# Optimization experiments

Hardware: AMD Instinct MI355X
Metric: run time of the kernel (lower is better)

## Reference

```python
import jax, jax.numpy as jnp
import numpy as np

B, S, E, H = 4, 2048, 768, 12
D = E // H  # head_dim = 64


def setup_inputs() -> dict:
    key = jax.random.key(0)
    k1, k2, k3 = jax.random.split(key, 3)
    x = jax.random.normal(k1, (B, S, E), dtype=jnp.float32)
    # torch Linear(E, 3E): weight [3E, E]; we store transposed [E, 3E] for x @ W
    W_qkv = jax.random.normal(k2, (E, 3 * E), dtype=jnp.float32) * (E ** -0.5)
    b_qkv = jax.random.normal(k3, (3 * E,), dtype=jnp.float32) * 0.02
    return {"x": x, "W_qkv": W_qkv, "b_qkv": b_qkv}


def reference(x, W_qkv, b_qkv):
    n, length, embed_dim = x.shape
    qkv = x @ W_qkv + b_qkv                                   # [B, S, 3E]
    qkv = qkv.reshape(n, length, 3, H, D).transpose(2, 0, 3, 1, 4)  # [3, B, H, S, D]
    q, k, v = qkv[0], qkv[1], qkv[2]
    scores = jnp.einsum('bhsd,bhtd->bhst', q, k) * (D ** -0.5)  # [B, H, S, S]
    attn = jax.nn.softmax(scores, axis=-1)
    out = jnp.einsum('bhst,bhtd->bhsd', attn, v)               # [B, H, S, D]
    return out.transpose(0, 2, 1, 3).reshape(n, length, embed_dim)
```

## Files before the change

### kernel.cpp

```cpp
#include <hip/hip_runtime.h>
#include <cmath>

#define B_ 4
#define S_ 2048
#define E_ 768
#define H_ 12
#define D_ 64
#define NE3 (3*E_)
#define QKV_ELEMS ((size_t)B_*H_*S_*D_)

typedef __attribute__((ext_vector_type(8)))  short bf16x8;
typedef __attribute__((ext_vector_type(4)))  float f32x4;
typedef __attribute__((ext_vector_type(16))) float f32x16;

__device__ __forceinline__ unsigned short f2bf(float f) {
    union { float f; unsigned u; } v; v.f = f;
    return (unsigned short)((v.u + 0x7FFFu + ((v.u >> 16) & 1u)) >> 16);
}
__device__ __forceinline__ float exp2_fast(float x) {
    float r; asm("v_exp_f32 %0, %1" : "=v"(r) : "v"(x)); return r;
}
__device__ __forceinline__ float max3f(float a, float b, float c) {
    float r; asm("v_max3_f32 %0, %1, %2, %3" : "=v"(r) : "v"(a), "v"(b), "v"(c));
    return r;
}
#define LOG2E 1.44269504088896340736f

__global__ __launch_bounds__(256)
void cvt_x(const float* __restrict__ x, unsigned short* __restrict__ xb)
{
    const size_t i = ((size_t)blockIdx.x * 256 + threadIdx.x) * 8;
    float4 a = *(const float4*)(x + i);
    float4 b = *(const float4*)(x + i + 4);
    ushort4 o0, o1;
    o0.x = f2bf(a.x); o0.y = f2bf(a.y); o0.z = f2bf(a.z); o0.w = f2bf(a.w);
    o1.x = f2bf(b.x); o1.y = f2bf(b.y); o1.z = f2bf(b.z); o1.w = f2bf(b.w);
    *(ushort4*)(xb + i)     = o0;
    *(ushort4*)(xb + i + 4) = o1;
}

__global__ __launch_bounds__(256)
void transpose_w(const float* __restrict__ W, unsigned short* __restrict__ Wt)
{
    __shared__ float t[32][33];
    const int tx = threadIdx.x & 31;
    const int ty = threadIdx.x >> 5;
    const int n0 = blockIdx.x * 32;
    const int k0 = blockIdx.y * 32;
    #pragma unroll
    for (int r = 0; r < 4; ++r)
        t[ty + 8*r][tx] = W[(size_t)(k0 + ty + 8*r) * NE3 + n0 + tx];
    __syncthreads();
    #pragma unroll
    for (int r = 0; r < 4; ++r)
        Wt[(size_t)(n0 + ty + 8*r) * E_ + k0 + tx] = f2bf(t[tx][ty + 8*r]);
}

__global__ __launch_bounds__(256, 2)
void qkv_gemm_mfma(const unsigned short* __restrict__ xb,
                   const unsigned short* __restrict__ Wt,
                   const float* __restrict__ bias,
                   unsigned short* __restrict__ qkv)
{
    __shared__ __align__(16) unsigned short As[128*64];
    __shared__ __align__(16) unsigned short Bs[128*64];

    const int tid  = threadIdx.x;
    const int lane = tid & 63;
    const int wave = tid >> 6;
    const int lo   = lane & 15;
    const int hi   = lane >> 4;
    const int wr   = wave >> 1;
    const int wc   = wave & 1;
    const int nstart = blockIdx.x * 128;
    const int mstart = blockIdx.y * 128;

    f32x4 acc[4][4];
    #pragma unroll
    for (int i = 0; i < 4; ++i)
        #pragma unroll
        for (int j = 0; j < 4; ++j) acc[i][j] = (f32x4){0.f,0.f,0.f,0.f};

    for (int k0 = 0; k0 < E_; k0 += 64) {
        __syncthreads();
        #pragma unroll
        for (int it = 0; it < 4; ++it) {
            const int cid = tid + it*256;
            const int row = cid >> 3, c = cid & 7;
            bf16x8 av = *(const bf16x8*)(xb + (size_t)(mstart + row)*E_ + k0 + c*8);
            *(bf16x8*)&As[row*64 + ((c ^ (row & 7)) * 8)] = av;
            bf16x8 bv = *(const bf16x8*)(Wt + (size_t)(nstart + row)*E_ + k0 + c*8);
            *(bf16x8*)&Bs[row*64 + ((c ^ (row & 7)) * 8)] = bv;
        }
        __syncthreads();

        #pragma unroll
        for (int ks = 0; ks < 2; ++ks) {
            const int c = ks*4 + hi;
            bf16x8 af[4], bfr[4];
            #pragma unroll
            for (int i = 0; i < 4; ++i) {
                const int ar = wr*64 + i*16 + lo;
                af[i] = *(const bf16x8*)&As[ar*64 + ((c ^ (ar & 7)) * 8)];
            }
            #pragma unroll
            for (int j = 0; j < 4; ++j) {
                const int br = wc*64 + j*16 + lo;
                bfr[j] = *(const bf16x8*)&Bs[br*64 + ((c ^ (br & 7)) * 8)];
            }
            #pragma unroll
            for (int i = 0; i < 4; ++i)
                #pragma unroll
                for (int j = 0; j < 4; ++j)
                    acc[i][j] = __builtin_amdgcn_mfma_f32_16x16x32_bf16(
                        af[i], bfr[j], acc[i][j], 0, 0, 0);
        }
    }

    #pragma unroll
    for (int j = 0; j < 4; ++j) {
        const int ncol = nstart + wc*64 + j*16 + lo;
        const int g  = ncol >> 6;
        const int cq = g / H_;
        const int h  = g % H_;
        const int d  = ncol & 63;
        const float bv = bias[ncol];
        const float qscale = (cq == 0) ? 0.125f : 1.0f;
        unsigned short* dst = qkv + (size_t)cq * QKV_ELEMS;
        #pragma unroll
        for (int i = 0; i < 4; ++i) {
            const int mbase = mstart + wr*64 + i*16 + hi*4;
            #pragma unroll
            for (int r = 0; r < 4; ++r) {
                const int m = mbase + r;
                const int b = m >> 11;
                const int s = m & 2047;
                dst[(((size_t)(b*H_ + h))*S_ + s)*D_ + d] =
                    f2bf((acc[i][j][r] + bv) * qscale);
            }
        }
    }
}

__global__ __launch_bounds__(256, 2)
void attn_mfma32(const unsigned short* __restrict__ qkv, float* __restrict__ out)
{
    __shared__ __align__(16) unsigned short Ks[2*64*64];
    __shared__ __align__(16) unsigned short Vt[2*64*64];

    const int tid  = threadIdx.x;
    const int lane = tid & 63;
    const int wave = tid >> 6;
    const int q32  = lane & 31;
    const int hi   = lane >> 5;
    const int qtile = blockIdx.x * 128;
    const int bh = blockIdx.y;
    const size_t base = (size_t)bh * S_ * D_;

    const unsigned short* Q = qkv;
    const unsigned short* K = qkv + QKV_ELEMS;
    const unsigned short* V = qkv + 2*QKV_ELEMS;

    bf16x8 qf[4];
    {
        const size_t qrow = base + (size_t)(qtile + wave*32 + q32) * D_;
        #pragma unroll
        for (int m = 0; m < 4; ++m)
            qf[m] = *(const bf16x8*)(Q + qrow + m*16 + hi*8);
    }

    const int kkey0 = tid >> 3,          kch0 = tid & 7;
    const int kkey1 = (tid + 256) >> 3,  kch1 = (tid + 256) & 7;

    bf16x8 vreg0, vreg1;
    #define GLOADK(kc_, buf_) do {                                                   \
        __builtin_amdgcn_global_load_lds(                                            \
            (const __attribute__((address_space(1))) unsigned*)                      \
                (K + base + (size_t)((kc_) + kkey0)*D_ + ((kch0 ^ (kkey0 & 7))*8)),  \
            (__attribute__((address_space(3))) unsigned*)&Ks[(buf_)*4096 + tid*8],   \
            16, 0, 0);                                                               \
        __builtin_amdgcn_global_load_lds(                                            \
            (const __attribute__((address_space(1))) unsigned*)                      \
                (K + base + (size_t)((kc_) + kkey1)*D_ + ((kch1 ^ (kkey1 & 7))*8)),  \
            (__attribute__((address_space(3))) unsigned*)&Ks[(buf_)*4096 + (tid+256)*8], \
            16, 0, 0);                                                               \
    } while (0)
    #define LOADV(kc_) do {                                                          \
        vreg0 = *(const bf16x8*)(V + base + (size_t)((kc_) + lane)*D_ + wave*16);    \
        vreg1 = *(const bf16x8*)(V + base + (size_t)((kc_) + lane)*D_ + wave*16 + 8);\
    } while (0)
    #define STOREV(buf_) do {                                                        \
        const int o_ = (buf_) * 4096;                                                \
        _Pragma("unroll")                                                            \
        for (int j = 0; j < 8; ++j) {                                                \
            const int d = wave*16 + j;                                               \
            Vt[o_ + d*64 + (((lane >> 3) ^ (d & 7)) * 8) + (lane & 7)] =             \
                (unsigned short)vreg0[j];                                            \
        }                                                                            \
        _Pragma("unroll")                                                            \
        for (int j = 0; j < 8; ++j) {                                                \
            const int d = wave*16 + 8 + j;                                           \
            Vt[o_ + d*64 + (((lane >> 3) ^ (d & 7)) * 8) + (lane & 7)] =             \
                (unsigned short)vreg1[j];                                            \
        }                                                                            \
    } while (0)

    f32x16 o0, o1;
    #pragma unroll
    for (int r = 0; r < 16; ++r) { o0[r] = 0.f; o1[r] = 0.f; }
    float m_run = -INFINITY, l_run = 0.f;

    GLOADK(0, 0);
    LOADV(0);
    STOREV(0);
    __syncthreads();
    int cur = 0;

    for (int kc = 0; kc < S_; kc += 64) {
        const int nkc = (kc + 64 < S_) ? (kc + 64) : 0;
        GLOADK(nkc, cur ^ 1);
        LOADV(nkc);

        const int o = cur * 4096;

        f32x16 sg[2];
        __builtin_amdgcn_s_setprio(1);
        #pragma unroll
        for (int g = 0; g < 2; ++g) {
            f32x16 acc;
            #pragma unroll
            for (int r = 0; r < 16; ++r) acc[r] = 0.f;
            const int key = g*32 + q32;
            #pragma unroll
            for (int m = 0; m < 4; ++m) {
                const int c = m*2 + hi;
                bf16x8 kf = *(const bf16x8*)&Ks[o + key*64 + ((c ^ (key & 7)) * 8)];
                acc = __builtin_amdgcn_mfma_f32_32x32x16_bf16(kf, qf[m], acc, 0, 0, 0);
            }
            sg[g] = acc;
        }
        __builtin_amdgcn_s_setprio(0);

        float m0 = fmaxf(sg[0][0], sg[0][1]);
        float m1 = fmaxf(sg[0][8], sg[0][9]);
        float m2 = fmaxf(sg[1][0], sg[1][1]);
        float m3 = fmaxf(sg[1][8], sg[1][9]);
        #pragma unroll
        for (int r = 2; r < 8; r += 2) {
            m0 = max3f(m0, sg[0][r],   sg[0][r+1]);
            m1 = max3f(m1, sg[0][r+8], sg[0][r+9]);
            m2 = max3f(m2, sg[1][r],   sg[1][r+1]);
            m3 = max3f(m3, sg[1][r+8], sg[1][r+9]);
        }
        float mx = fmaxf(fmaxf(m0, m1), fmaxf(m2, m3));
        mx = fmaxf(mx, __shfl_xor(mx, 32));

        if (__any(mx > m_run + 8.0f)) {
            const float mn    = fmaxf(m_run, mx);
            const float alpha = exp2_fast((m_run - mn) * LOG2E);
            m_run = mn;
            l_run *= alpha;
            #pragma unroll
            for (int r = 0; r < 16; ++r) { o0[r] *= alpha; o1[r] *= alpha; }
        }
        const float nmnL = -m_run * LOG2E;

        #pragma unroll
        for (int r = 0; r < 16; ++r) sg[0][r] = exp2_fast(fmaf(sg[0][r], LOG2E, nmnL));
        #pragma unroll
        for (int r = 0; r < 16; ++r) sg[1][r] = exp2_fast(fmaf(sg[1][r], LOG2E, nmnL));

        float a8[8];
        #pragma unroll
        for (int r = 0; r < 8; ++r) a8[r] = (sg[0][r] + sg[0][r+8]) + (sg[1][r] + sg[1][r+8]);
        float a4_0 = a8[0] + a8[4], a4_1 = a8[1] + a8[5];
        float a4_2 = a8[2] + a8[6], a4_3 = a8[3] + a8[7];
        float psum = (a4_0 + a4_1) + (a4_2 + a4_3);
        psum += __shfl_xor(psum, 32);
        l_run += psum;

        unsigned U0[8], U1[8];
        #pragma unroll
        for (int c2 = 0; c2 < 8; ++c2) {
            asm("v_cvt_pk_bf16_f32 %0, %1, %2"
                : "=v"(U0[c2]) : "v"(sg[0][2*c2]), "v"(sg[0][2*c2+1]));
            asm("v_cvt_pk_bf16_f32 %0, %1, %2"
                : "=v"(U1[c2]) : "v"(sg[1][2*c2]), "v"(sg[1][2*c2+1]));
        }

        unsigned R0[2][2], R1[2][2];
        #pragma unroll
        for (int tb = 0; tb < 2; ++tb)
            #pragma unroll
            for (int w2 = 0; w2 < 2; ++w2) {
                unsigned s0 = hi ? U0[4*tb + w2] : U0[4*tb + 2 + w2];
                unsigned s1 = hi ? U1[4*tb + w2] : U1[4*tb + 2 + w2];
                R0[tb][w2] = (unsigned)__shfl_xor((int)s0, 32);
                R1[tb][w2] = (unsigned)__shfl_xor((int)s1, 32);
            }

        __builtin_amdgcn_s_setprio(1);
        #pragma unroll
        for (int t = 0; t < 4; ++t) {
            const int tb = t & 1;
            union { unsigned w[4]; bf16x8 v; } pw;
            if (t < 2) {
                pw.w[0] = hi ? R0[tb][0] : U0[4*tb + 0];
                pw.w[1] = hi ? R0[tb][1] : U0[4*tb + 1];
                pw.w[2] = hi ? U0[4*tb + 2] : R0[tb][0];
                pw.w[3] = hi ? U0[4*tb + 3] : R0[tb][1];
            } else {
                pw.w[0] = hi ? R1[tb][0] : U1[4*tb + 0];
                pw.w[1] = hi ? R1[tb][1] : U1[4*tb + 1];
                pw.w[2] = hi ? U1[4*tb + 2] : R1[tb][0];
                pw.w[3] = hi ? U1[4*tb + 3] : R1[tb][1];
            }
            const int c = t*2 + hi;
            {
                const int d = q32;
                bf16x8 vf = *(const bf16x8*)&Vt[o + d*64 + ((c ^ (d & 7)) * 8)];
                o0 = __builtin_amdgcn_mfma_f32_32x32x16_bf16(vf, pw.v, o0, 0, 0, 0);
            }
            {
                const int d = 32 + q32;
                bf16x8 vf = *(const bf16x8*)&Vt[o + d*64 + ((c ^ (d & 7)) * 8)];
                o1 = __builtin_amdgcn_mfma_f32_32x32x16_bf16(vf, pw.v, o1, 0, 0, 0);
            }
        }
        __builtin_amdgcn_s_setprio(0);

        STOREV(cur ^ 1);
        __syncthreads();
        cur ^= 1;
    }

    const int b = bh / H_;
    const int h = bh % H_;
    const float inv = 1.f / l_run;
    const int qglob = qtile + wave*32 + q32;
    float* obase = out + ((size_t)b*S_ + qglob)*E_ + h*64;
    #pragma unroll
    for (int rg = 0; rg < 4; ++rg) {
        float4 w0 = { o0[4*rg+0]*inv, o0[4*rg+1]*inv, o0[4*rg+2]*inv, o0[4*rg+3]*inv };
        *(float4*)(obase + rg*8 + hi*4) = w0;
        float4 w1 = { o1[4*rg+0]*inv, o1[4*rg+1]*inv, o1[4*rg+2]*inv, o1[4*rg+3]*inv };
        *(float4*)(obase + 32 + rg*8 + hi*4) = w1;
    }
    #undef GLOADK
    #undef LOADV
    #undef STOREV
}

extern "C" void kernel_launch(void* const* d_in, const int* in_sizes, int n_in,
                              void* d_out, int out_size, void* d_ws, size_t ws_size,
                              hipStream_t stream)
{
    (void)in_sizes; (void)n_in; (void)out_size; (void)ws_size;
    const float* x    = (const float*)d_in[0];
    const float* W    = (const float*)d_in[1];
    const float* bias = (const float*)d_in[2];
    float* out = (float*)d_out;

    unsigned short* qkv = (unsigned short*)d_ws;
    unsigned short* xb  = qkv + 3*QKV_ELEMS;
    unsigned short* Wtb = xb + (size_t)B_*S_*E_;

    cvt_x<<<(B_*S_*E_)/(256*8), 256, 0, stream>>>(x, xb);
    transpose_w<<<dim3(NE3/32, E_/32), 256, 0, stream>>>(W, Wtb);

    dim3 g1(NE3/128, (B_*S_)/128);
    qkv_gemm_mfma<<<g1, 256, 0, stream>>>(xb, Wtb, bias, qkv);

    dim3 g2(S_/128, B_*H_);
    attn_mfma32<<<g2, 256, 0, stream>>>(qkv, out);
}
```

Before: 138.4 us.

## Write V transposed from QKV GEMM and stream it to LDS asynchronously

The QKV GEMM epilogue now writes V in a [bh, d, s] transposed layout to a separate workspace buffer using 4-wide stores. The attention kernel then loads the V tile straight into LDS with global_load_lds, the same way it loads K. This removes the per-iteration register round trip and the scalar LDS transpose stores for V. It uses extra workspace, and the GEMM now writes V with strided 8-byte stores.

After: 138.6 us. About the same (+0.2%).

```diff
diff --git a/kernel.cpp b/kernel.cpp
--- a/kernel.cpp
+++ b/kernel.cpp
@@ -60,7 +60,8 @@
 void qkv_gemm_mfma(const unsigned short* __restrict__ xb,
                    const unsigned short* __restrict__ Wt,
                    const float* __restrict__ bias,
-                   unsigned short* __restrict__ qkv)
+                   unsigned short* __restrict__ qkv,
+                   unsigned short* __restrict__ vtg)
 {
     __shared__ __align__(16) unsigned short As[128*64];
     __shared__ __align__(16) unsigned short Bs[128*64];
@@ -130,20 +131,29 @@
         #pragma unroll
         for (int i = 0; i < 4; ++i) {
             const int mbase = mstart + wr*64 + i*16 + hi*4;
-            #pragma unroll
-            for (int r = 0; r < 4; ++r) {
-                const int m = mbase + r;
-                const int b = m >> 11;
-                const int s = m & 2047;
-                dst[(((size_t)(b*H_ + h))*S_ + s)*D_ + d] =
-                    f2bf((acc[i][j][r] + bv) * qscale);
+            const int b  = mbase >> 11;
+            const int s0 = mbase & 2047;
+            if (cq == 2) {
+                ushort4 vv;
+                vv.x = f2bf(acc[i][j][0] + bv);
+                vv.y = f2bf(acc[i][j][1] + bv);
+                vv.z = f2bf(acc[i][j][2] + bv);
+                vv.w = f2bf(acc[i][j][3] + bv);
+                *(ushort4*)(vtg + (((size_t)(b*H_ + h))*D_ + d)*S_ + s0) = vv;
+            } else {
+                #pragma unroll
+                for (int r = 0; r < 4; ++r)
+                    dst[(((size_t)(b*H_ + h))*S_ + s0 + r)*D_ + d] =
+                        f2bf((acc[i][j][r] + bv) * qscale);
             }
         }
     }
 }
 
 __global__ __launch_bounds__(256, 2)
-void attn_mfma32(const unsigned short* __restrict__ qkv, float* __restrict__ out)
+void attn_mfma32(const unsigned short* __restrict__ qkv,
+                 const unsigned short* __restrict__ vtg,
+                 float* __restrict__ out)
 {
     __shared__ __align__(16) unsigned short Ks[2*64*64];
     __shared__ __align__(16) unsigned short Vt[2*64*64];
@@ -155,11 +165,11 @@
     const int hi   = lane >> 5;
     const int qtile = blockIdx.x * 128;
     const int bh = blockIdx.y;
-    const size_t base = (size_t)bh * S_ * D_;
+    const size_t base  = (size_t)bh * S_ * D_;
+    const size_t baseT = (size_t)bh * D_ * S_;
 
     const unsigned short* Q = qkv;
     const unsigned short* K = qkv + QKV_ELEMS;
-    const unsigned short* V = qkv + 2*QKV_ELEMS;
 
     bf16x8 qf[4];
     {
@@ -171,8 +181,9 @@
 
     const int kkey0 = tid >> 3,          kch0 = tid & 7;
     const int kkey1 = (tid + 256) >> 3,  kch1 = (tid + 256) & 7;
-
-    bf16x8 vreg0, vreg1;
+    const int vd0 = tid >> 3, vs0 = tid & 7;
+    const int vd1 = vd0 + 32;
+
     #define GLOADK(kc_, buf_) do {                                                   \
         __builtin_amdgcn_global_load_lds(                                            \
             (const __attribute__((address_space(1))) unsigned*)                      \
@@ -185,24 +196,17 @@
             (__attribute__((address_space(3))) unsigned*)&Ks[(buf_)*4096 + (tid+256)*8], \
             16, 0, 0);                                                               \
     } while (0)
-    #define LOADV(kc_) do {                                                          \
-        vreg0 = *(const bf16x8*)(V + base + (size_t)((kc_) + lane)*D_ + wave*16);    \
-        vreg1 = *(const bf16x8*)(V + base + (size_t)((kc_) + lane)*D_ + wave*16 + 8);\
-    } while (0)
-    #define STOREV(buf_) do {                                                        \
-        const int o_ = (buf_) * 4096;                                                \
-        _Pragma("unroll")                                                            \
-        for (int j = 0; j < 8; ++j) {                                                \
-            const int d = wave*16 + j;                                               \
-            Vt[o_ + d*64 + (((lane >> 3) ^ (d & 7)) * 8) + (lane & 7)] =             \
-                (unsigned short)vreg0[j];                                            \
-        }                                                                            \
-        _Pragma("unroll")                                                            \
-        for (int j = 0; j < 8; ++j) {                                                \
-            const int d = wave*16 + 8 + j;                                           \
-            Vt[o_ + d*64 + (((lane >> 3) ^ (d & 7)) * 8) + (lane & 7)] =             \
-                (unsigned short)vreg1[j];                                            \
-        }                                                                            \
+    #define GLOADV(kc_, buf_) do {                                                   \
+        __builtin_amdgcn_global_load_lds(                                            \
+            (const __attribute__((address_space(1))) unsigned*)                      \
+                (vtg + baseT + (size_t)vd0*S_ + (kc_) + ((vs0 ^ (vd0 & 7))*8)),      \
+            (__attribute__((address_space(3))) unsigned*)&Vt[(buf_)*4096 + tid*8],   \
+            16, 0, 0);                                                               \
+        __builtin_amdgcn_global_load_lds(                                            \
+            (const __attribute__((address_space(1))) unsigned*)                      \
+                (vtg + baseT + (size_t)vd1*S_ + (kc_) + ((vs0 ^ (vd1 & 7))*8)),      \
+            (__attribute__((address_space(3))) unsigned*)&Vt[(buf_)*4096 + (tid+256)*8], \
+            16, 0, 0);                                                               \
     } while (0)
 
     f32x16 o0, o1;
@@ -211,15 +215,14 @@
     float m_run = -INFINITY, l_run = 0.f;
 
     GLOADK(0, 0);
-    LOADV(0);
-    STOREV(0);
+    GLOADV(0, 0);
     __syncthreads();
     int cur = 0;
 
     for (int kc = 0; kc < S_; kc += 64) {
         const int nkc = (kc + 64 < S_) ? (kc + 64) : 0;
         GLOADK(nkc, cur ^ 1);
-        LOADV(nkc);
+        GLOADV(nkc, cur ^ 1);
 
         const int o = cur * 4096;
 
@@ -329,7 +332,6 @@
         }
         __builtin_amdgcn_s_setprio(0);
 
-        STOREV(cur ^ 1);
         __syncthreads();
         cur ^= 1;
     }
@@ -347,8 +349,7 @@
         *(float4*)(obase + 32 + rg*8 + hi*4) = w1;
     }
     #undef GLOADK
-    #undef LOADV
-    #undef STOREV
+    #undef GLOADV
 }
 
 extern "C" void kernel_launch(void* const* d_in, const int* in_sizes, int n_in,
@@ -364,13 +365,14 @@
     unsigned short* qkv = (unsigned short*)d_ws;
     unsigned short* xb  = qkv + 3*QKV_ELEMS;
     unsigned short* Wtb = xb + (size_t)B_*S_*E_;
+    unsigned short* vtg = Wtb + (size_t)E_*NE3;
 
     cvt_x<<<(B_*S_*E_)/(256*8), 256, 0, stream>>>(x, xb);
     transpose_w<<<dim3(NE3/32, E_/32), 256, 0, stream>>>(W, Wtb);
 
     dim3 g1(NE3/128, (B_*S_)/128);
-    qkv_gemm_mfma<<<g1, 256, 0, stream>>>(xb, Wtb, bias, qkv);
+    qkv_gemm_mfma<<<g1, 256, 0, stream>>>(xb, Wtb, bias, qkv, vtg);
 
     dim3 g2(S_/128, B_*H_);
-    attn_mfma32<<<g2, 256, 0, stream>>>(qkv, out);
-}
+    attn_mfma32<<<g2, 256, 0, stream>>>(qkv, vtg, out);
+}
```
